# Kernel tuning notes

Measured on AMD Instinct MI355X. Metric: run time of the kernel, lower is better.

The kernel has to match this reference:

```python
import jax, jax.numpy as jnp
import numpy as np


def setup_inputs() -> dict:
    key = jax.random.key(0)
    k1, k2 = jax.random.split(key)
    B, C, H = 1024, 1000, 512  # batch, classes, hidden
    y = jax.random.normal(k1, (B, C), dtype=jnp.float32)
    w = jax.random.normal(k2, (C, H), dtype=jnp.float32)
    epsilon = jnp.ones((), dtype=jnp.float32)
    lipschitz = jnp.ones((), dtype=jnp.float32)
    return {"y": y, "w": w, "epsilon": epsilon, "lipschitz": lipschitz}


def reference(y, w, epsilon, lipschitz):
    # y: [B, C] logits; w: [C, H] final-layer weight
    kW = lipschitz * w.T                      # [H, C]
    j = jnp.argmax(y, axis=1)                 # [B]
    y_j = jnp.max(y, axis=1, keepdims=True)   # [B, 1]
    kW_j = kW.T[j]                            # [B, H] gather of argmax column
    kW_ij = kW_j[:, :, None] - kW[None]       # [B, H, C] broadcast difference
    sq = jnp.sum(kW_ij * kW_ij, axis=1)       # [B, C]
    # safe sqrt (value identical; avoids NaN grad at the exact-zero j column)
    K_ij = jnp.where(sq > 0, jnp.sqrt(jnp.where(sq > 0, sq, 1.0)), 0.0)
    y_bot_i = y + epsilon * K_ij              # [B, C]
    y_bot_i = jnp.where(y == y_j, -jnp.inf, y_bot_i)
    y_bot = jnp.max(y_bot_i, axis=1, keepdims=True)  # [B, 1]
    return jnp.concatenate([y, y_bot], axis=1)       # [B, C+1]
```

## Files before the change

kernel.cpp:

```cpp
#include <hip/hip_runtime.h>
#include <math.h>

#define B_SZ 1024
#define C_SZ 1000
#define H_SZ 512


typedef __attribute__((ext_vector_type(8))) short bf16x8;
typedef __attribute__((ext_vector_type(4))) float f32x4;

__global__ __launch_bounds__(256) void k_prep(
    const float* __restrict__ y, const float* __restrict__ w,
    int* __restrict__ jv, float* __restrict__ ymax,
    float* __restrict__ wnorm, short* __restrict__ wbf,
    float* __restrict__ out) {
    const int r = blockIdx.x;
    const int tid = threadIdx.x;
    if (r < 250) {
        const int wave = tid >> 6, lane = tid & 63;
        const int c = r * 4 + wave;
        const float* row = w + c * H_SZ;
        float4 a = *(const float4*)(row + lane * 8);
        float4 b = *(const float4*)(row + lane * 8 + 4);
        float f[8] = {a.x, a.y, a.z, a.w, b.x, b.y, b.z, b.w};
        unsigned short u[8];
        float s = 0.f;
#pragma unroll
        for (int i = 0; i < 8; ++i) {
            s += f[i] * f[i];
            unsigned v = __float_as_uint(f[i]);
            v += 0x7fffu + ((v >> 16) & 1u);
            u[i] = (unsigned short)(v >> 16);
        }
        uint4 pk;
        pk.x = (unsigned)u[0] | ((unsigned)u[1] << 16);
        pk.y = (unsigned)u[2] | ((unsigned)u[3] << 16);
        pk.z = (unsigned)u[4] | ((unsigned)u[5] << 16);
        pk.w = (unsigned)u[6] | ((unsigned)u[7] << 16);
        *(uint4*)(wbf + c * H_SZ + lane * 8) = pk;
#pragma unroll
        for (int off = 32; off; off >>= 1) s += __shfl_down(s, off, 64);
        if (lane == 0) wnorm[c] = s;
    } else {
        const int b = r - 250;
        const float* yrow = y + b * C_SZ;
        float* orow = out + b * (C_SZ + 1);
        float best = -INFINITY;
        int bidx = 0x7fffffff;
        if (tid < 250) {
            float4 v = *(const float4*)(yrow + tid * 4);
            float e[4] = {v.x, v.y, v.z, v.w};
#pragma unroll
            for (int i = 0; i < 4; ++i) {
                orow[tid * 4 + i] = e[i];
                if (e[i] > best) { best = e[i]; bidx = tid * 4 + i; }
            }
        }
        const int lane = tid & 63;
#pragma unroll
        for (int off = 32; off; off >>= 1) {
            float ov = __shfl_down(best, off, 64);
            int oi = __shfl_down(bidx, off, 64);
            if (ov > best || (ov == best && oi < bidx)) { best = ov; bidx = oi; }
        }
        __shared__ float sv[4];
        __shared__ int si[4];
        if (lane == 0) { sv[tid >> 6] = best; si[tid >> 6] = bidx; }
        __syncthreads();
        if (tid == 0) {
            float bv = sv[0]; int bi = si[0];
#pragma unroll
            for (int k = 1; k < 4; ++k) {
                if (sv[k] > bv || (sv[k] == bv && si[k] < bi)) { bv = sv[k]; bi = si[k]; }
            }
            jv[b] = bi;
            ymax[b] = bv;
        }
    }
}

__global__ __launch_bounds__(256) void k_main(
    const float* __restrict__ y, const short* __restrict__ wbf,
    const float* __restrict__ eps_p, const float* __restrict__ lip_p,
    const int* __restrict__ jv, const float* __restrict__ ymax,
    const float* __restrict__ wnorm, float* __restrict__ part) {
    const int t = threadIdx.x;
    const int wave = t >> 6, lane = t & 63;
    const int col = lane & 15, quad = lane >> 4;
    const int by = blockIdx.y, bx = blockIdx.x;
    const int b0 = by * 32 + (wave >> 1) * 16;
    const int half = wave & 1;
    const int c0 = bx * 32 + half * 16;

    const int arow = jv[b0 + col];
    const int ccol = c0 + col;
    const int crow = ccol < C_SZ ? ccol : C_SZ - 1;
    const short* ap = wbf + arow * H_SZ + quad * 8;
    const short* bp = wbf + crow * H_SZ + quad * 8;

    f32x4 acc = {0.f, 0.f, 0.f, 0.f};
    bf16x8 acur = *(const bf16x8*)ap;
    bf16x8 bcur = *(const bf16x8*)bp;
#pragma unroll
    for (int it = 0; it < 15; ++it) {
        bf16x8 anx = *(const bf16x8*)(ap + (it + 1) * 32);
        bf16x8 bnx = *(const bf16x8*)(bp + (it + 1) * 32);
        acc = __builtin_amdgcn_mfma_f32_16x16x32_bf16(acur, bcur, acc, 0, 0, 0);
        acur = anx;
        bcur = bnx;
    }
    acc = __builtin_amdgcn_mfma_f32_16x16x32_bf16(acur, bcur, acc, 0, 0, 0);

    const float eps = *eps_p;
    const float L = *lip_p;
    const float L2 = L * L;
    const float nc = wnorm[crow];
    float rmax[4];
#pragma unroll
    for (int i = 0; i < 4; ++i) {
        const int b = b0 + quad * 4 + i;
        const float nj = wnorm[jv[b]];
        const float ym = ymax[b];
        float cand = -INFINITY;
        if (ccol < C_SZ) {
            const float yv = y[b * C_SZ + ccol];
            const float sq = L2 * (nj + nc - 2.0f * acc[i]);
            const float K = sq > 0.f ? sqrtf(sq) : 0.f;
            cand = (yv == ym) ? -INFINITY : yv + eps * K;
        }
        rmax[i] = cand;
    }
#pragma unroll
    for (int off = 8; off; off >>= 1)
#pragma unroll
        for (int i = 0; i < 4; ++i)
            rmax[i] = fmaxf(rmax[i], __shfl_xor(rmax[i], off, 64));
    if (col == 0) {
        float* slice = part + (bx * 2 + half) * B_SZ;
#pragma unroll
        for (int i = 0; i < 4; ++i)
            slice[b0 + quad * 4 + i] = rmax[i];
    }
}

__global__ void k_final(const float* __restrict__ part,
                        float* __restrict__ out) {
    int b = blockIdx.x * 256 + threadIdx.x;
    if (b >= B_SZ) return;
    float m = -INFINITY;
#pragma unroll
    for (int s = 0; s < 64; ++s) m = fmaxf(m, part[s * B_SZ + b]);
    out[b * (C_SZ + 1) + C_SZ] = m;
}

extern "C" void kernel_launch(void* const* d_in, const int* in_sizes, int n_in,
                              void* d_out, int out_size, void* d_ws,
                              size_t ws_size, hipStream_t stream) {
    const float* y = (const float*)d_in[0];
    const float* w = (const float*)d_in[1];
    const float* eps = (const float*)d_in[2];
    const float* lip = (const float*)d_in[3];
    float* out = (float*)d_out;

    char* ws = (char*)d_ws;
    int* jv = (int*)ws;
    float* ymax = (float*)(ws + 4096);
    float* wnorm = (float*)(ws + 8192);
    float* part = (float*)(ws + 16384);
    short* wbf = (short*)(ws + 524288);

    k_prep<<<250 + B_SZ, 256, 0, stream>>>(y, w, jv, ymax, wnorm, wbf, out);
    k_main<<<dim3(32, 32), 256, 0, stream>>>(y, wbf, eps, lip, jv, ymax, wnorm,
                                             part);
    k_final<<<(B_SZ + 255) / 256, 256, 0, stream>>>(part, out);
}
```

Before: 84.52 us.

## Tile k_main as 64x64 blocks with LDS-staged bf16 operands and register prefetch

Replaces the per-wave 16x16 tiles, which loaded A and B straight from global memory, with 64x64 block tiles. Operands are staged through padded shared memory in 128-wide K chunks, with the next chunk prefetched into registers, and each wave reuses its A fragment across four column tiles. This cuts redundant global and L2 traffic and shrinks the partial-max buffer from 64 slices to 16. The cost is a grid of only 256 blocks, fewer than the CU count on MI355X, plus extra LDS use and two barriers per chunk.

Measured after the change: 82.66 us. 1.02x faster.

```diff
diff --git a/kernel.cpp b/kernel.cpp
--- a/kernel.cpp
+++ b/kernel.cpp
@@ -79,56 +79,109 @@
     }
 }
 
+#define KC 128
+#define RS 136
 __global__ __launch_bounds__(256) void k_main(
     const float* __restrict__ y, const short* __restrict__ wbf,
     const float* __restrict__ eps_p, const float* __restrict__ lip_p,
     const int* __restrict__ jv, const float* __restrict__ ymax,
     const float* __restrict__ wnorm, float* __restrict__ part) {
+    __shared__ __align__(16) short As[64 * RS];
+    __shared__ __align__(16) short Bs[64 * RS];
+    __shared__ int sjv[64];
+    __shared__ float snj[64];
+    __shared__ float sym[64];
+
     const int t = threadIdx.x;
-    const int wave = t >> 6, lane = t & 63;
+    const int bx = blockIdx.x, by = blockIdx.y;
+    const int b0 = by * 64, c0 = bx * 64;
+
+    if (t < 64) {
+        int j = jv[b0 + t];
+        sjv[t] = j;
+        snj[t] = wnorm[j];
+        sym[t] = ymax[b0 + t];
+    }
+    __syncthreads();
+
+    const int srow = t >> 2;
+    const int sseg = t & 3;
+    int crow = c0 + srow; if (crow > C_SZ - 1) crow = C_SZ - 1;
+    const short* agsrc = wbf + sjv[srow] * H_SZ;
+    const short* bgsrc = wbf + crow * H_SZ;
+
+    uint4 pa[4], pb[4];
+#pragma unroll
+    for (int p = 0; p < 4; ++p) {
+        const int off = (sseg + p * 4) * 8;
+        pa[p] = *(const uint4*)(agsrc + off);
+        pb[p] = *(const uint4*)(bgsrc + off);
+    }
+
+    const int wv = t >> 6, lane = t & 63;
     const int col = lane & 15, quad = lane >> 4;
-    const int by = blockIdx.y, bx = blockIdx.x;
-    const int b0 = by * 32 + (wave >> 1) * 16;
-    const int half = wave & 1;
-    const int c0 = bx * 32 + half * 16;
-
-    const int arow = jv[b0 + col];
-    const int ccol = c0 + col;
-    const int crow = ccol < C_SZ ? ccol : C_SZ - 1;
-    const short* ap = wbf + arow * H_SZ + quad * 8;
-    const short* bp = wbf + crow * H_SZ + quad * 8;
-
-    f32x4 acc = {0.f, 0.f, 0.f, 0.f};
-    bf16x8 acur = *(const bf16x8*)ap;
-    bf16x8 bcur = *(const bf16x8*)bp;
-#pragma unroll
-    for (int it = 0; it < 15; ++it) {
-        bf16x8 anx = *(const bf16x8*)(ap + (it + 1) * 32);
-        bf16x8 bnx = *(const bf16x8*)(bp + (it + 1) * 32);
-        acc = __builtin_amdgcn_mfma_f32_16x16x32_bf16(acur, bcur, acc, 0, 0, 0);
-        acur = anx;
-        bcur = bnx;
-    }
-    acc = __builtin_amdgcn_mfma_f32_16x16x32_bf16(acur, bcur, acc, 0, 0, 0);
+    const short* ard = &As[(wv * 16 + col) * RS + quad * 8];
+    const short* brd = &Bs[col * RS + quad * 8];
+
+    f32x4 acc[4] = {{0.f, 0.f, 0.f, 0.f},
+                    {0.f, 0.f, 0.f, 0.f},
+                    {0.f, 0.f, 0.f, 0.f},
+                    {0.f, 0.f, 0.f, 0.f}};
+
+    for (int ch = 0; ch < 4; ++ch) {
+#pragma unroll
+        for (int p = 0; p < 4; ++p) {
+            const int off = (sseg + p * 4) * 8;
+            *(uint4*)&As[srow * RS + off] = pa[p];
+            *(uint4*)&Bs[srow * RS + off] = pb[p];
+        }
+        __syncthreads();
+        if (ch < 3) {
+            const int gbase = (ch + 1) * KC;
+#pragma unroll
+            for (int p = 0; p < 4; ++p) {
+                const int off = gbase + (sseg + p * 4) * 8;
+                pa[p] = *(const uint4*)(agsrc + off);
+                pb[p] = *(const uint4*)(bgsrc + off);
+            }
+        }
+#pragma unroll
+        for (int ks = 0; ks < 4; ++ks) {
+            bf16x8 af = *(const bf16x8*)(ard + ks * 32);
+#pragma unroll
+            for (int ct = 0; ct < 4; ++ct) {
+                bf16x8 bf = *(const bf16x8*)(brd + ct * 16 * RS + ks * 32);
+                acc[ct] =
+                    __builtin_amdgcn_mfma_f32_16x16x32_bf16(af, bf, acc[ct], 0, 0, 0);
+            }
+        }
+        __syncthreads();
+    }
 
     const float eps = *eps_p;
     const float L = *lip_p;
     const float L2 = L * L;
-    const float nc = wnorm[crow];
     float rmax[4];
 #pragma unroll
     for (int i = 0; i < 4; ++i) {
-        const int b = b0 + quad * 4 + i;
-        const float nj = wnorm[jv[b]];
-        const float ym = ymax[b];
-        float cand = -INFINITY;
-        if (ccol < C_SZ) {
-            const float yv = y[b * C_SZ + ccol];
-            const float sq = L2 * (nj + nc - 2.0f * acc[i]);
-            const float K = sq > 0.f ? sqrtf(sq) : 0.f;
-            cand = (yv == ym) ? -INFINITY : yv + eps * K;
-        }
-        rmax[i] = cand;
+        const int br = wv * 16 + quad * 4 + i;
+        const int b = b0 + br;
+        const float nj = snj[br];
+        const float ym = sym[br];
+        float m = -INFINITY;
+#pragma unroll
+        for (int ct = 0; ct < 4; ++ct) {
+            const int cc = c0 + ct * 16 + col;
+            if (cc < C_SZ) {
+                const float yv = y[b * C_SZ + cc];
+                const float nc = wnorm[cc];
+                const float sq = L2 * (nj + nc - 2.0f * acc[ct][i]);
+                const float K = sq > 0.f ? sqrtf(sq) : 0.f;
+                const float cand = (yv == ym) ? -INFINITY : yv + eps * K;
+                m = fmaxf(m, cand);
+            }
+        }
+        rmax[i] = m;
     }
 #pragma unroll
     for (int off = 8; off; off >>= 1)
@@ -136,10 +189,10 @@
         for (int i = 0; i < 4; ++i)
             rmax[i] = fmaxf(rmax[i], __shfl_xor(rmax[i], off, 64));
     if (col == 0) {
-        float* slice = part + (bx * 2 + half) * B_SZ;
+        float* slice = part + bx * B_SZ;
 #pragma unroll
         for (int i = 0; i < 4; ++i)
-            slice[b0 + quad * 4 + i] = rmax[i];
+            slice[b0 + wv * 16 + quad * 4 + i] = rmax[i];
     }
 }
 
@@ -149,7 +202,7 @@
     if (b >= B_SZ) return;
     float m = -INFINITY;
 #pragma unroll
-    for (int s = 0; s < 64; ++s) m = fmaxf(m, part[s * B_SZ + b]);
+    for (int s = 0; s < 16; ++s) m = fmaxf(m, part[s * B_SZ + b]);
     out[b * (C_SZ + 1) + C_SZ] = m;
 }
 
@@ -170,7 +223,7 @@
     short* wbf = (short*)(ws + 524288);
 
     k_prep<<<250 + B_SZ, 256, 0, stream>>>(y, w, jv, ymax, wnorm, wbf, out);
-    k_main<<<dim3(32, 32), 256, 0, stream>>>(y, wbf, eps, lip, jv, ymax, wnorm,
+    k_main<<<dim3(16, 16), 256, 0, stream>>>(y, wbf, eps, lip, jv, ymax, wnorm,
                                              part);
     k_final<<<(B_SZ + 255) / 256, 256, 0, stream>>>(part, out);
 }
```
